# Optimization experiments

Measured on AMD Instinct MI355X. Metric: run time of the kernel, lower is better.

The kernel has to match this reference:

```python
import jax, jax.numpy as jnp
import numpy as np

W_CHAMFER = 1.0
W_SMOOTH = 0.5
K_NEIGHBORS = 8


def _pairwise_sqdist(a, b):
    # a: [B,N,3], b: [B,M,3] -> [B,N,M] squared euclidean distances
    a2 = jnp.sum(a * a, axis=-1)  # [B,N]
    b2 = jnp.sum(b * b, axis=-1)  # [B,M]
    ab = jnp.einsum('bnd,bmd->bnm', a, b)  # [B,N,M]
    d2 = a2[:, :, None] + b2[:, None, :] - 2.0 * ab
    return jnp.maximum(d2, 0.0)


def _chamfer(pc1, pc2):
    d = jnp.sqrt(_pairwise_sqdist(pc1, pc2))  # [B,N,M] euclidean (matches torch.norm)
    d1 = jnp.min(d, axis=2)  # [B,N]
    d2 = jnp.min(d, axis=1)  # [B,M]
    return jnp.mean(d1) + jnp.mean(d2)


def _smoothness(pc, flow, k=K_NEIGHBORS):
    d2 = _pairwise_sqdist(pc, pc)  # [B,N,N]
    # k+1 nearest (squared dist preserves ordering); drop self (index 0)
    _, idx = jax.lax.top_k(-d2, k + 1)  # [B,N,k+1]
    idx = idx[:, :, 1:]  # [B,N,k]
    neighbor_flow = jax.vmap(lambda f, i: f[i])(flow, idx)  # [B,N,k,3]
    diff = flow[:, :, None, :] - neighbor_flow
    return jnp.mean(jnp.linalg.norm(diff, axis=-1))


def setup_inputs() -> dict:
    key = jax.random.key(0)
    k1, k2, k3 = jax.random.split(key, 3)
    B, N, M = 2, 8192, 8192
    pc1 = jax.random.normal(k1, (B, N, 3), dtype=jnp.float32)
    pc2 = jax.random.normal(k2, (B, M, 3), dtype=jnp.float32)
    pred_flow = jax.random.normal(k3, (B, N, 3), dtype=jnp.float32) * 0.1
    return {"pc1": pc1, "pc2": pc2, "pred_flow": pred_flow}


def reference(pc1, pc2, pred_flow):
    pc1_warped = pc1 + pred_flow
    l_chamfer = _chamfer(pc1_warped, pc2)
    l_smooth = _smoothness(pc1, pred_flow)
    return W_CHAMFER * l_chamfer + W_SMOOTH * l_smooth
```

## Files before the change

kernel.cpp:

```cpp
#include <hip/hip_runtime.h>

#define N_PTS 8192
#define BATCH 2
#define KNN 8
#define STILE 1024
#define NBLK_C 1024
#define NBLK_S 1024
#define NBLOCKS (NBLK_C + NBLK_S)

__device__ __forceinline__ void ce(unsigned &x, unsigned &y) {
    unsigned lo = min(x, y), hi = max(x, y); x = lo; y = hi;
}

__device__ __forceinline__ void insert4(unsigned o[4], unsigned key) {
    unsigned n0 = min(o[0], key);
    unsigned n1 = max(o[0], min(o[1], key));
    unsigned n2 = max(o[1], min(o[2], key));
    unsigned n3 = max(o[2], min(o[3], key));
    o[0]=n0; o[1]=n1; o[2]=n2; o[3]=n3;
}

__device__ __forceinline__ void merge_stage8(unsigned m[8], int d) {
    unsigned p[8], c[8];
    #pragma unroll
    for (int k = 0; k < 8; ++k) p[k] = (unsigned)__shfl_xor((int)m[k], d, 64);
    #pragma unroll
    for (int k = 0; k < 8; ++k) c[k] = min(m[k], p[7-k]);
    ce(c[0],c[4]); ce(c[1],c[5]); ce(c[2],c[6]); ce(c[3],c[7]);
    ce(c[0],c[2]); ce(c[1],c[3]); ce(c[4],c[6]); ce(c[5],c[7]);
    ce(c[0],c[1]); ce(c[2],c[3]); ce(c[4],c[5]); ce(c[6],c[7]);
    #pragma unroll
    for (int k = 0; k < 8; ++k) m[k] = c[k];
}

__device__ __forceinline__ void merge64(unsigned m[8]) {
    merge_stage8(m, 1); merge_stage8(m, 2); merge_stage8(m, 4);
    merge_stage8(m, 8); merge_stage8(m, 16); merge_stage8(m, 32);
}

__global__ __launch_bounds__(256, 4) void mega_kernel(
        const float* __restrict__ pc1, const float* __restrict__ pc2,
        const float* __restrict__ flow, float* __restrict__ out) {
    __shared__ float4 sq[STILE];
    __shared__ float psum[4];
    const int tid = threadIdx.x;
    const int bx = blockIdx.x;
    const int lane = tid & 63, wv = tid >> 6;

    if (bx < NBLK_C) {
        const int z  = bx >> 8;
        const int bb = z & 1, dir = z >> 1;
        const int cb = bx & 255;
        const float* P1 = pc1  + (size_t)bb * N_PTS * 3;
        const float* P2 = pc2  + (size_t)bb * N_PTS * 3;
        const float* FL = flow + (size_t)bb * N_PTS * 3;
        const int sub = tid & 15;
        const int r0 = cb * 32 + (tid >> 4) * 2;

        float mx0, my0, mz0, p20, mx1, my1, mz1, p21;
        {
            float px, py, pz;
            if (dir == 0) {
                px = P1[r0*3+0] + FL[r0*3+0];
                py = P1[r0*3+1] + FL[r0*3+1];
                pz = P1[r0*3+2] + FL[r0*3+2];
            } else {
                px = P2[r0*3+0]; py = P2[r0*3+1]; pz = P2[r0*3+2];
            }
            mx0 = -2.0f * px; my0 = -2.0f * py; mz0 = -2.0f * pz;
            p20 = fmaf(px, px, fmaf(py, py, pz * pz));
            const int r1 = r0 + 1;
            if (dir == 0) {
                px = P1[r1*3+0] + FL[r1*3+0];
                py = P1[r1*3+1] + FL[r1*3+1];
                pz = P1[r1*3+2] + FL[r1*3+2];
            } else {
                px = P2[r1*3+0]; py = P2[r1*3+1]; pz = P2[r1*3+2];
            }
            mx1 = -2.0f * px; my1 = -2.0f * py; mz1 = -2.0f * pz;
            p21 = fmaf(px, px, fmaf(py, py, pz * pz));
        }
        float b0 = __builtin_inff(), b1 = __builtin_inff();

        #pragma unroll 1
        for (int tile = 0; tile < N_PTS / STILE; ++tile) {
            const int t0 = tile * STILE;
            __syncthreads();
            #pragma unroll
            for (int u = tid; u < STILE; u += 256) {
                int g = t0 + u;
                float qx, qy, qz;
                if (dir == 0) {
                    qx = P2[g*3+0]; qy = P2[g*3+1]; qz = P2[g*3+2];
                } else {
                    qx = P1[g*3+0] + FL[g*3+0];
                    qy = P1[g*3+1] + FL[g*3+1];
                    qz = P1[g*3+2] + FL[g*3+2];
                }
                sq[u] = make_float4(qx, qy, qz, fmaf(qx, qx, fmaf(qy, qy, qz * qz)));
            }
            __syncthreads();

            #pragma unroll 8
            for (int c = 0; c < STILE / 16; c += 2) {
                float4 qa = sq[c * 16 + sub];
                float4 qb = sq[c * 16 + 16 + sub];
                float s0a = fmaf(mx0, qa.x, fmaf(my0, qa.y, fmaf(mz0, qa.z, qa.w)));
                float s1a = fmaf(mx1, qa.x, fmaf(my1, qa.y, fmaf(mz1, qa.z, qa.w)));
                float s0b = fmaf(mx0, qb.x, fmaf(my0, qb.y, fmaf(mz0, qb.z, qb.w)));
                float s1b = fmaf(mx1, qb.x, fmaf(my1, qb.y, fmaf(mz1, qb.z, qb.w)));
                b0 = fminf(fminf(b0, s0a), s0b);
                b1 = fminf(fminf(b1, s1a), s1b);
            }
        }

        #pragma unroll
        for (int d = 1; d <= 8; d <<= 1) {
            b0 = fminf(b0, __shfl_xor(b0, d, 64));
            b1 = fminf(b1, __shfl_xor(b1, d, 64));
        }
        float val = ((lane & 15) == 0)
            ? (sqrtf(fmaxf(b0 + p20, 0.0f)) + sqrtf(fmaxf(b1 + p21, 0.0f)))
            : 0.0f;
        #pragma unroll
        for (int d = 1; d < 64; d <<= 1) val += __shfl_xor(val, d, 64);
        if (lane == 0) psum[wv] = val;
        __syncthreads();

        if (tid == 0) {
            float ch = psum[0] + psum[1] + psum[2] + psum[3];
            atomicAdd(out, ch * (1.0f / (float)(BATCH * N_PTS)));
        }
    } else {
        const int sx9 = bx - NBLK_C;
        const int b  = sx9 >> 9;
        const int sx = sx9 & 511;
        const int i0w = sx * 16 + wv * 4;
        const float* P = pc1  + (size_t)b * N_PTS * 3;
        const float* F = flow + (size_t)b * N_PTS * 3;

        float mx[4], my[4], mz[4], p2[4], gr[4];
        unsigned thr[4], o[4][4];
        #pragma unroll
        for (int r = 0; r < 4; ++r) {
            int i = i0w + r;
            float px = P[i*3+0], py = P[i*3+1], pz = P[i*3+2];
            mx[r] = -2.0f * px; my[r] = -2.0f * py; mz[r] = -2.0f * pz;
            p2[r] = fmaf(px, px, fmaf(py, py, pz * pz));
            gr[r] = __builtin_inff();
            thr[r] = 0xFFFFFFFFu;
            #pragma unroll
            for (int k = 0; k < 4; ++k) o[r][k] = 0xFFFFFFFFu;
        }

        auto update_thr = [&]() {
            #pragma unroll
            for (int r = 0; r < 4; ++r) {
                unsigned m0 = o[r][0], m1 = o[r][1], m2 = o[r][2], m3 = o[r][3];
                #pragma unroll
                for (int d = 1; d <= 16; d <<= 1) {
                    unsigned q0 = (unsigned)__shfl_xor((int)m0, d, 64);
                    unsigned q1 = (unsigned)__shfl_xor((int)m1, d, 64);
                    unsigned q2 = (unsigned)__shfl_xor((int)m2, d, 64);
                    unsigned q3 = (unsigned)__shfl_xor((int)m3, d, 64);
                    unsigned c0 = min(m0, q3), c1 = min(m1, q2);
                    unsigned c2 = min(m2, q1), c3 = min(m3, q0);
                    ce(c0, c2); ce(c1, c3); ce(c0, c1); ce(c2, c3);
                    m0 = c0; m1 = c1; m2 = c2; m3 = c3;
                }
                unsigned bound = max(m3, (unsigned)__shfl_xor((int)m3, 32, 64));
                thr[r] = min(thr[r], bound);
                float thr_up = __uint_as_float((thr[r] & 0xFFFFE000u) + 0x4000u);
                gr[r] = thr_up - p2[r];
            }
        };

        auto gated_span = [&](int t0, int st0, int st1) {
            #pragma unroll 2
            for (int st = st0; st < st1; ++st) {
                float4 qa = sq[st * 64 + lane];
                int j = t0 + st * 64 + lane;
                float sc[4];
                #pragma unroll
                for (int r = 0; r < 4; ++r)
                    sc[r] = fmaf(mx[r], qa.x, fmaf(my[r], qa.y, fmaf(mz[r], qa.z, qa.w)));
                #pragma unroll
                for (int r = 0; r < 4; ++r) {
                    if (__any(sc[r] <= gr[r])) {
                        float d2 = fmaxf(sc[r] + p2[r], 0.0f);
                        unsigned key = (__float_as_uint(d2) & 0xFFFFE000u) | (unsigned)j;
                        key = (j == i0w + r) ? 0xFFFFFFFFu : key;
                        insert4(o[r], key);
                    }
                }
            }
        };

        #pragma unroll 1
        for (int tile = 0; tile < N_PTS / STILE; ++tile) {
            const int t0 = tile * STILE;
            __syncthreads();
            #pragma unroll
            for (int u = tid; u < STILE; u += 256) {
                int g = t0 + u;
                float qx = P[g*3+0], qy = P[g*3+1], qz = P[g*3+2];
                sq[u] = make_float4(qx, qy, qz, fmaf(qx, qx, fmaf(qy, qy, qz * qz)));
            }
            __syncthreads();

            if (tile == 0) {
                #pragma unroll 4
                for (int st = 0; st < STILE / 64; ++st) {
                    float4 qa = sq[st * 64 + lane];
                    int j = st * 64 + lane;
                    #pragma unroll
                    for (int r = 0; r < 4; ++r) {
                        float ss = fmaf(mx[r], qa.x, fmaf(my[r], qa.y, fmaf(mz[r], qa.z, qa.w)));
                        float d2 = fmaxf(ss + p2[r], 0.0f);
                        unsigned key = (__float_as_uint(d2) & 0xFFFFE000u) | (unsigned)j;
                        key = (j == i0w + r) ? 0xFFFFFFFFu : key;
                        insert4(o[r], key);
                    }
                }
                update_thr();
            } else {
                gated_span(t0, 0, STILE / 64);
                if (tile == 1 || tile == 3) update_thr();
            }
        }

        const int sel = lane & 31;
        const int pr = sel >> 3, kk = sel & 7;
        unsigned mykey = 0xFFFFFFFFu;
        #pragma unroll
        for (int r = 0; r < 4; ++r) {
            unsigned m[8] = {o[r][0], o[r][1], o[r][2], o[r][3],
                             0xFFFFFFFFu, 0xFFFFFFFFu, 0xFFFFFFFFu, 0xFFFFFFFFu};
            merge64(m);
            if (pr == r) {
                unsigned k2 = m[0];
                #pragma unroll
                for (int t = 1; t < 8; ++t) k2 = (kk == t) ? m[t] : k2;
                mykey = k2;
            }
        }
        const int i = i0w + pr;
        const int j = (int)(mykey & (N_PTS - 1));
        float dx = F[i*3+0] - F[j*3+0];
        float dy = F[i*3+1] - F[j*3+1];
        float dz = F[i*3+2] - F[j*3+2];
        float sv = sqrtf(fmaf(dx, dx, fmaf(dy, dy, dz * dz)));
        #pragma unroll
        for (int d = 1; d < 64; d <<= 1) sv += __shfl_xor(sv, d, 64);
        if (lane == 0) psum[wv] = sv;
        __syncthreads();

        if (tid == 0) {
            float sm = psum[0] + psum[1] + psum[2] + psum[3];
            atomicAdd(out, sm * (0.25f / ((float)BATCH * N_PTS * KNN)));
        }
    }
}

extern "C" void kernel_launch(void* const* d_in, const int* in_sizes, int n_in,
                              void* d_out, int out_size, void* d_ws, size_t ws_size,
                              hipStream_t stream) {
    const float* pc1  = (const float*)d_in[0];
    const float* pc2  = (const float*)d_in[1];
    const float* flow = (const float*)d_in[2];
    float* out = (float*)d_out;

    mega_kernel<<<dim3(NBLOCKS), 256, 0, stream>>>(pc1, pc2, flow, out);
}
```

Measured before the change: 135.5 us.

## Remap chamfer work so each wave owns 8 query rows and lanes split candidates

In the chamfer branch, each wave now handles 8 query points held in registers, and each lane scans a distinct candidate from shared memory. Before, 16-lane groups each handled two query rows. Every shared-memory float4 load is now reused across 8 rows instead of 2, which cuts LDS traffic per FMA. The cost is a full 64-lane min-reduction for each of the 8 rows at the end, plus higher register pressure.

After: 134.5 us. No clear change (-0.8%).

```diff
diff --git a/kernel.cpp b/kernel.cpp
--- a/kernel.cpp
+++ b/kernel.cpp
@@ -54,33 +54,23 @@
         const float* P1 = pc1  + (size_t)bb * N_PTS * 3;
         const float* P2 = pc2  + (size_t)bb * N_PTS * 3;
         const float* FL = flow + (size_t)bb * N_PTS * 3;
-        const int sub = tid & 15;
-        const int r0 = cb * 32 + (tid >> 4) * 2;
-
-        float mx0, my0, mz0, p20, mx1, my1, mz1, p21;
-        {
+        const int rbase = cb * 32 + wv * 8;
+
+        float mx[8], my[8], mz[8], bmin[8];
+        #pragma unroll
+        for (int k = 0; k < 8; ++k) {
+            const int r = rbase + k;
             float px, py, pz;
             if (dir == 0) {
-                px = P1[r0*3+0] + FL[r0*3+0];
-                py = P1[r0*3+1] + FL[r0*3+1];
-                pz = P1[r0*3+2] + FL[r0*3+2];
+                px = P1[r*3+0] + FL[r*3+0];
+                py = P1[r*3+1] + FL[r*3+1];
+                pz = P1[r*3+2] + FL[r*3+2];
             } else {
-                px = P2[r0*3+0]; py = P2[r0*3+1]; pz = P2[r0*3+2];
-            }
-            mx0 = -2.0f * px; my0 = -2.0f * py; mz0 = -2.0f * pz;
-            p20 = fmaf(px, px, fmaf(py, py, pz * pz));
-            const int r1 = r0 + 1;
-            if (dir == 0) {
-                px = P1[r1*3+0] + FL[r1*3+0];
-                py = P1[r1*3+1] + FL[r1*3+1];
-                pz = P1[r1*3+2] + FL[r1*3+2];
-            } else {
-                px = P2[r1*3+0]; py = P2[r1*3+1]; pz = P2[r1*3+2];
-            }
-            mx1 = -2.0f * px; my1 = -2.0f * py; mz1 = -2.0f * pz;
-            p21 = fmaf(px, px, fmaf(py, py, pz * pz));
-        }
-        float b0 = __builtin_inff(), b1 = __builtin_inff();
+                px = P2[r*3+0]; py = P2[r*3+1]; pz = P2[r*3+2];
+            }
+            mx[k] = -2.0f * px; my[k] = -2.0f * py; mz[k] = -2.0f * pz;
+            bmin[k] = __builtin_inff();
+        }
 
         #pragma unroll 1
         for (int tile = 0; tile < N_PTS / STILE; ++tile) {
@@ -101,30 +91,34 @@
             }
             __syncthreads();
 
-            #pragma unroll 8
-            for (int c = 0; c < STILE / 16; c += 2) {
-                float4 qa = sq[c * 16 + sub];
-                float4 qb = sq[c * 16 + 16 + sub];
-                float s0a = fmaf(mx0, qa.x, fmaf(my0, qa.y, fmaf(mz0, qa.z, qa.w)));
-                float s1a = fmaf(mx1, qa.x, fmaf(my1, qa.y, fmaf(mz1, qa.z, qa.w)));
-                float s0b = fmaf(mx0, qb.x, fmaf(my0, qb.y, fmaf(mz0, qb.z, qb.w)));
-                float s1b = fmaf(mx1, qb.x, fmaf(my1, qb.y, fmaf(mz1, qb.z, qb.w)));
-                b0 = fminf(fminf(b0, s0a), s0b);
-                b1 = fminf(fminf(b1, s1a), s1b);
-            }
-        }
-
-        #pragma unroll
-        for (int d = 1; d <= 8; d <<= 1) {
-            b0 = fminf(b0, __shfl_xor(b0, d, 64));
-            b1 = fminf(b1, __shfl_xor(b1, d, 64));
-        }
-        float val = ((lane & 15) == 0)
-            ? (sqrtf(fmaxf(b0 + p20, 0.0f)) + sqrtf(fmaxf(b1 + p21, 0.0f)))
-            : 0.0f;
-        #pragma unroll
-        for (int d = 1; d < 64; d <<= 1) val += __shfl_xor(val, d, 64);
-        if (lane == 0) psum[wv] = val;
+            #pragma unroll 2
+            for (int c = 0; c < STILE / 64; c += 2) {
+                float4 qa = sq[c * 64 + lane];
+                float4 qb = sq[c * 64 + 64 + lane];
+                #pragma unroll
+                for (int k = 0; k < 8; ++k) {
+                    float sa = fmaf(mx[k], qa.x, fmaf(my[k], qa.y, fmaf(mz[k], qa.z, qa.w)));
+                    float sb = fmaf(mx[k], qb.x, fmaf(my[k], qb.y, fmaf(mz[k], qb.z, qb.w)));
+                    bmin[k] = fminf(fminf(bmin[k], sa), sb);
+                }
+            }
+        }
+
+        #pragma unroll
+        for (int k = 0; k < 8; ++k) {
+            #pragma unroll
+            for (int d = 1; d < 64; d <<= 1)
+                bmin[k] = fminf(bmin[k], __shfl_xor(bmin[k], d, 64));
+        }
+        if (lane == 0) {
+            float val = 0.0f;
+            #pragma unroll
+            for (int k = 0; k < 8; ++k) {
+                float p2k = 0.25f * fmaf(mx[k], mx[k], fmaf(my[k], my[k], mz[k] * mz[k]));
+                val += sqrtf(fmaxf(bmin[k] + p2k, 0.0f));
+            }
+            psum[wv] = val;
+        }
         __syncthreads();
 
         if (tid == 0) {
```
